# Performance work log

Measured on AMD Instinct MI355X. Metric: run time of the kernel, lower is better.

## Reference

```python
import jax, jax.numpy as jnp
import numpy as np

RADIUS = 0.5
BATCH, N, C_IN, C_OUT = 8, 1024, 64, 64


def setup_inputs() -> dict:
    key = jax.random.key(0)
    k1, k2, k3 = jax.random.split(key, 3)
    features = jax.random.normal(k1, (BATCH, N, C_IN), dtype=jnp.float32)
    geometry = jax.random.normal(k2, (BATCH, N, 3), dtype=jnp.float32)
    # Kernel stand-in: linear map from relative position to [C_out, C_in] matrix
    W = jax.random.normal(k3, (3, C_OUT, C_IN), dtype=jnp.float32) / np.sqrt(3.0 * C_IN)
    return {"features": features, "geometry": geometry, "W": W}


def reference(features, geometry, W):
    # diff[z,a,b,:] = r_b - r_a  (neighbor minus center), matching rb - ra in torch
    diff = geometry[:, None, :, :] - geometry[:, :, None, :]          # [z,a,b,3]
    norm = jnp.sqrt(jnp.sum(diff * diff, axis=-1))                    # [z,a,b]
    # rel_mask: 1 where within radius (the dense equivalent of the padded
    # neighbor-list + mask; padded/out-of-ball entries contribute zero)
    rel_mask = (norm < RADIUS).astype(features.dtype)                 # [z,a,b]
    # kernel(diff)[z,a,b,i,j] = sum_x diff[z,a,b,x] * W[x,i,j]
    # output[z,a,i] = sum_{b,x,j} mask*diff[z,a,b,x] * W[x,i,j] * feat[z,b,j]
    mdiff = rel_mask[..., None] * diff                                # [z,a,b,3]
    tmp = jnp.einsum('zabx,zbj->zaxj', mdiff, features)               # [z,a,3,Cin]
    out = jnp.einsum('zaxj,xij->zai', tmp, W)                         # [z,a,Cout]
    return out
```

## Files before the change

kernel.cpp:

```cpp
#include <hip/hip_runtime.h>


#define BATCHSZ 8
#define NPTS 1024
#define CIN 64
#define COUT 64
#define NXJ (3 * CIN)
#define NG (NXJ / 4)
#define WPB 16
#define BS (WPB * 64)
#define GPW (NG / 8)
#define NSTEP (NPTS / 64)

typedef float f32x2 __attribute__((ext_vector_type(2)));

#define SM_WS 3072
#define SM_TOTAL 15360

__global__ __launch_bounds__(BS, 8) void neigh_conv_kernel(
    const float* __restrict__ feat,
    const float* __restrict__ geom,
    const float* __restrict__ W,
    float* __restrict__ out)
{
    const int lane = threadIdx.x & 63;
    const int wv   = threadIdx.x >> 6;
    const int h    = wv >> 3;
    const int hw   = wv & 7;
    const int p    = blockIdx.x * WPB + wv;
    const int a    = p & (NPTS - 1);
    const int z    = p >> 10;

    __shared__ __align__(16) float smem[SM_TOTAL];

    {
        const float4* gsrc = (const float4*)(geom + (size_t)z * NPTS * 3);
        float4* gdst = (float4*)smem;
        if (threadIdx.x < NPTS * 3 / 4)
            gdst[threadIdx.x] = gsrc[threadIdx.x];

        const float4* w4 = (const float4*)W;
        float4* ws = (float4*)(smem + SM_WS);
        #pragma unroll
        for (int kk = 0; kk < 3; ++kk) {
            const int k = threadIdx.x + kk * BS;
            const int idx = (k & ~15) | ((k + (k >> 4)) & 15);
            ws[idx] = w4[k];
        }
    }
    __syncthreads();

    const int g0 = hw * GPW;
    float4 wr[GPW];
    {
        const float4* ws = (const float4*)(smem + SM_WS);
        #pragma unroll
        for (int q = 0; q < GPW; ++q) {
            const int g = g0 + q;
            const int x = g >> 4, c = g & 15;
            wr[q] = ws[x * 1024 + (lane << 4) + ((c + lane) & 15)];
        }
    }

    const float* geo = smem;
    const float gax = geo[a * 3 + 0];
    const float gay = geo[a * 3 + 1];
    const float gaz = geo[a * 3 + 2];
    const float* fz = feat + (size_t)z * NPTS * CIN;

    unsigned long long masks[NSTEP];
    #pragma unroll
    for (int ss = 0; ss < NSTEP; ++ss) {
        const int b = ss * 64 + lane;
        float d2;
        {
            #pragma clang fp contract(off)
            const float dx = geo[b * 3 + 0] - gax;
            const float dy = geo[b * 3 + 1] - gay;
            const float dz = geo[b * 3 + 2] - gaz;
            d2 = dx * dx + dy * dy + dz * dz;
        }
        masks[ss] = __ballot(d2 < 0.25f);
    }

    float acc0 = 0.f, acc1 = 0.f, acc2 = 0.f;
    int   b1 = -1, b2 = -1;
    float f1 = 0.f, f2 = 0.f;

    auto consume = [&](int bc, float fc) {
        const float gbx = geo[bc * 3 + 0];
        const float gby = geo[bc * 3 + 1];
        const float gbz = geo[bc * 3 + 2];
        const float dx = gbx - gax;
        const float dy = gby - gay;
        const float dz = gbz - gaz;
        acc0 = fmaf(dx, fc, acc0);
        acc1 = fmaf(dy, fc, acc1);
        acc2 = fmaf(dz, fc, acc2);
    };

    #pragma unroll
    for (int ss = 0; ss < NSTEP; ++ss) {
        unsigned long long mm = masks[ss];
        while (mm) {
            const int src = __ffsll(mm) - 1;
            mm &= mm - 1ull;
            const int b = ss * 64 + src;
            const float f = fz[(size_t)b * CIN + lane];
            if (b2 >= 0) consume(b2, f2);
            b2 = b1; f2 = f1;
            b1 = b;  f1 = f;
        }
    }
    if (b2 >= 0) consume(b2, f2);
    if (b1 >= 0) consume(b1, f1);

    __syncthreads();

    float* tmp = smem + wv * NXJ;
    tmp[0 * CIN + lane] = acc0;
    tmp[1 * CIN + lane] = acc1;
    tmp[2 * CIN + lane] = acc2;
    __syncthreads();

    float* red = smem + SM_WS + h * (8 * 8 * COUT);
    #pragma unroll
    for (int pp = 0; pp < 8; ++pp) {
        const float4* t4 = (const float4*)(smem + (h * 8 + pp) * NXJ);
        f32x2 facc = {0.f, 0.f};
        #pragma unroll
        for (int q = 0; q < GPW; ++q) {
            const float4 t = t4[g0 + q];
            f32x2 ta; ta.x = t.x; ta.y = t.y;
            f32x2 tb; tb.x = t.z; tb.y = t.w;
            f32x2 wa; wa.x = wr[q].x; wa.y = wr[q].y;
            f32x2 wb; wb.x = wr[q].z; wb.y = wr[q].w;
            facc = ta * wa + facc;
            facc = tb * wb + facc;
        }
        red[(hw * 8 + pp) * COUT + lane] = facc.x + facc.y;
    }
    __syncthreads();

    float o = 0.f;
    #pragma unroll
    for (int w = 0; w < 8; ++w)
        o += red[(w * 8 + hw) * COUT + lane];

    out[(size_t)p * COUT + lane] = o;
}

extern "C" void kernel_launch(void* const* d_in, const int* in_sizes, int n_in,
                              void* d_out, int out_size, void* d_ws, size_t ws_size,
                              hipStream_t stream) {
    const float* feat = (const float*)d_in[0];
    const float* geom = (const float*)d_in[1];
    const float* W    = (const float*)d_in[2];
    float* out        = (float*)d_out;

    const int nblocks = BATCHSZ * NPTS / WPB;
    neigh_conv_kernel<<<nblocks, BS, 0, stream>>>(feat, geom, W, out);
}
```

Baseline: 18.08 us.

## Read geometry from global, broadcast neighbor offsets via readlane, drop LDS geometry staging

Geometry is no longer staged into shared memory. Each lane loads its candidate neighbor's coordinates directly from global memory, and the mask ballot is fused into the neighbor-consume loop. Offsets for each accepted neighbor are broadcast with readlane instead of being re-read from LDS. The per-wave temp buffer moves to a separate LDS region, which removes one __syncthreads; the trade-off is 16 uncoalesced strided global geometry loads per wave and serial readlane overhead.

```diff
diff --git a/kernel.cpp b/kernel.cpp
--- a/kernel.cpp
+++ b/kernel.cpp
@@ -14,7 +14,7 @@
 
 typedef float f32x2 __attribute__((ext_vector_type(2)));
 
-#define SM_WS 3072
+#define SM_TMP 12288
 #define SM_TOTAL 15360
 
 __global__ __launch_bounds__(BS, 8) void neigh_conv_kernel(
@@ -34,13 +34,8 @@
     __shared__ __align__(16) float smem[SM_TOTAL];
 
     {
-        const float4* gsrc = (const float4*)(geom + (size_t)z * NPTS * 3);
-        float4* gdst = (float4*)smem;
-        if (threadIdx.x < NPTS * 3 / 4)
-            gdst[threadIdx.x] = gsrc[threadIdx.x];
-
         const float4* w4 = (const float4*)W;
-        float4* ws = (float4*)(smem + SM_WS);
+        float4* ws = (float4*)smem;
         #pragma unroll
         for (int kk = 0; kk < 3; ++kk) {
             const int k = threadIdx.x + kk * BS;
@@ -53,7 +48,7 @@
     const int g0 = hw * GPW;
     float4 wr[GPW];
     {
-        const float4* ws = (const float4*)(smem + SM_WS);
+        const float4* ws = (const float4*)smem;
         #pragma unroll
         for (int q = 0; q < GPW; ++q) {
             const int g = g0 + q;
@@ -62,71 +57,67 @@
         }
     }
 
-    const float* geo = smem;
-    const float gax = geo[a * 3 + 0];
-    const float gay = geo[a * 3 + 1];
-    const float gaz = geo[a * 3 + 2];
+    const float* gz = geom + (size_t)z * NPTS * 3;
     const float* fz = feat + (size_t)z * NPTS * CIN;
+    const float gax = gz[a * 3 + 0];
+    const float gay = gz[a * 3 + 1];
+    const float gaz = gz[a * 3 + 2];
 
-    unsigned long long masks[NSTEP];
+    float acc0 = 0.f, acc1 = 0.f, acc2 = 0.f;
+    float px1 = 0.f, py1 = 0.f, pz1 = 0.f, pf1 = 0.f;
+    float px2 = 0.f, py2 = 0.f, pz2 = 0.f, pf2 = 0.f;
+    int   v1 = 0, v2 = 0;
+
     #pragma unroll
     for (int ss = 0; ss < NSTEP; ++ss) {
         const int b = ss * 64 + lane;
-        float d2;
+        float dx, dy, dz, d2;
         {
             #pragma clang fp contract(off)
-            const float dx = geo[b * 3 + 0] - gax;
-            const float dy = geo[b * 3 + 1] - gay;
-            const float dz = geo[b * 3 + 2] - gaz;
+            dx = gz[b * 3 + 0] - gax;
+            dy = gz[b * 3 + 1] - gay;
+            dz = gz[b * 3 + 2] - gaz;
             d2 = dx * dx + dy * dy + dz * dz;
         }
-        masks[ss] = __ballot(d2 < 0.25f);
-    }
-
-    float acc0 = 0.f, acc1 = 0.f, acc2 = 0.f;
-    int   b1 = -1, b2 = -1;
-    float f1 = 0.f, f2 = 0.f;
-
-    auto consume = [&](int bc, float fc) {
-        const float gbx = geo[bc * 3 + 0];
-        const float gby = geo[bc * 3 + 1];
-        const float gbz = geo[bc * 3 + 2];
-        const float dx = gbx - gax;
-        const float dy = gby - gay;
-        const float dz = gbz - gaz;
-        acc0 = fmaf(dx, fc, acc0);
-        acc1 = fmaf(dy, fc, acc1);
-        acc2 = fmaf(dz, fc, acc2);
-    };
-
-    #pragma unroll
-    for (int ss = 0; ss < NSTEP; ++ss) {
-        unsigned long long mm = masks[ss];
+        unsigned long long mm = __ballot(d2 < 0.25f);
         while (mm) {
             const int src = __ffsll(mm) - 1;
             mm &= mm - 1ull;
-            const int b = ss * 64 + src;
-            const float f = fz[(size_t)b * CIN + lane];
-            if (b2 >= 0) consume(b2, f2);
-            b2 = b1; f2 = f1;
-            b1 = b;  f1 = f;
+            const int bn = ss * 64 + src;
+            const float nx = __int_as_float(__builtin_amdgcn_readlane(__float_as_int(dx), src));
+            const float ny = __int_as_float(__builtin_amdgcn_readlane(__float_as_int(dy), src));
+            const float nz = __int_as_float(__builtin_amdgcn_readlane(__float_as_int(dz), src));
+            const float f = fz[(size_t)bn * CIN + lane];
+            if (v2) {
+                acc0 = fmaf(px2, pf2, acc0);
+                acc1 = fmaf(py2, pf2, acc1);
+                acc2 = fmaf(pz2, pf2, acc2);
+            }
+            px2 = px1; py2 = py1; pz2 = pz1; pf2 = pf1; v2 = v1;
+            px1 = nx;  py1 = ny;  pz1 = nz;  pf1 = f;   v1 = 1;
         }
     }
-    if (b2 >= 0) consume(b2, f2);
-    if (b1 >= 0) consume(b1, f1);
+    if (v2) {
+        acc0 = fmaf(px2, pf2, acc0);
+        acc1 = fmaf(py2, pf2, acc1);
+        acc2 = fmaf(pz2, pf2, acc2);
+    }
+    if (v1) {
+        acc0 = fmaf(px1, pf1, acc0);
+        acc1 = fmaf(py1, pf1, acc1);
+        acc2 = fmaf(pz1, pf1, acc2);
+    }
 
-    __syncthreads();
-
-    float* tmp = smem + wv * NXJ;
+    float* tmp = smem + SM_TMP + wv * NXJ;
     tmp[0 * CIN + lane] = acc0;
     tmp[1 * CIN + lane] = acc1;
     tmp[2 * CIN + lane] = acc2;
     __syncthreads();
 
-    float* red = smem + SM_WS + h * (8 * 8 * COUT);
+    float* red = smem + h * (8 * 8 * COUT);
     #pragma unroll
     for (int pp = 0; pp < 8; ++pp) {
-        const float4* t4 = (const float4*)(smem + (h * 8 + pp) * NXJ);
+        const float4* t4 = (const float4*)(smem + SM_TMP + (h * 8 + pp) * NXJ);
         f32x2 facc = {0.f, 0.f};
         #pragma unroll
         for (int q = 0; q < GPW; ++q) {
```

Result: slower. 19.03 us (+5.3%).
